# Kernel optimization log

Hardware: AMD Instinct MI355X
Metric: run time of the kernel (lower is better)

Reference implementation:

```python
import jax, jax.numpy as jnp
import numpy as np

N_NODES = 100000
N_EDGES = 20000
NNZ = 1600000


def _hconv(x, node_idx, edge_idx, W, b):
    # PyG HypergraphConv (no attention): out = D^-1 H (B^-1 H^T (x W)) + b
    xw = x @ W  # [N, F_out]
    ones = jnp.ones((node_idx.shape[0],), dtype=x.dtype)
    Bdeg = jax.ops.segment_sum(ones, edge_idx, num_segments=N_EDGES)
    Binv = jnp.where(Bdeg > 0, 1.0 / Bdeg, 0.0)
    # node -> hyperedge aggregation
    e = jax.ops.segment_sum(xw[node_idx], edge_idx, num_segments=N_EDGES)
    e = e * Binv[:, None]
    Ddeg = jax.ops.segment_sum(ones, node_idx, num_segments=N_NODES)
    Dinv = jnp.where(Ddeg > 0, 1.0 / Ddeg, 0.0)
    # hyperedge -> node aggregation
    out = jax.ops.segment_sum(e[edge_idx], node_idx, num_segments=N_NODES)
    return out * Dinv[:, None] + b


def setup_inputs() -> dict:
    key = jax.random.key(0)
    ks = jax.random.split(key, 12)
    x = jax.random.normal(ks[0], (N_NODES, 300), dtype=jnp.float32)
    node_idx = jax.random.randint(ks[1], (NNZ,), 0, N_NODES)
    edge_idx = jax.random.randint(ks[2], (NNZ,), 0, N_EDGES)
    hyper_edge_index = jnp.stack([node_idx, edge_idx], axis=0)
    def lin(kw, kb, fi, fo):
        s = 1.0 / np.sqrt(fi)
        W = jax.random.uniform(kw, (fi, fo), jnp.float32, -s, s)
        b = jax.random.uniform(kb, (fo,), jnp.float32, -s, s)
        return W, b
    W1, b1 = lin(ks[3], ks[4], 300, 256)
    W2, b2 = lin(ks[5], ks[6], 256, 256)
    W3, b3 = lin(ks[7], ks[8], 256, 128)
    attn_W, attn_b = lin(ks[9], ks[10], 128, 1)
    return {"x": x, "hyper_edge_index": hyper_edge_index,
            "W1": W1, "b1": b1, "W2": W2, "b2": b2,
            "W3": W3, "b3": b3, "attn_W": attn_W, "attn_b": attn_b}


def reference(x, hyper_edge_index, W1, b1, W2, b2, W3, b3, attn_W, attn_b):
    node_idx = hyper_edge_index[0]
    edge_idx = hyper_edge_index[1]
    h = jax.nn.leaky_relu(_hconv(x, node_idx, edge_idx, W1, b1), negative_slope=0.01)
    # dropout is identity at inference
    h = jax.nn.leaky_relu(_hconv(h, node_idx, edge_idx, W2, b2), negative_slope=0.01)
    h = _hconv(h, node_idx, edge_idx, W3, b3)  # [N, 128]
    # attention pooling over all nodes (softmax along dim 0)
    logits = h @ attn_W + attn_b  # [N, 1]
    attn = jax.nn.softmax(logits, axis=0)
    return jnp.sum(attn * h, axis=0)  # [128]
```

## Files before the change

kernel.cpp:

```cpp
#include <hip/hip_runtime.h>
#include <hip/hip_bf16.h>
#include <string.h>

#define N_NODES 100000
#define N_EDGES 20000
#define NNZ     1600000

#define CHUNK   8192
#define NBE     157
#define NBN     391
#define NBLK_BIN ((NNZ + CHUNK - 1) / CHUNK)


__device__ __forceinline__ unsigned short f2bf(float f) {
    unsigned int u = __float_as_uint(f);
    unsigned int r = (u + 0x7fffu + ((u >> 16) & 1u)) >> 16;
    return (unsigned short)r;
}
__device__ __forceinline__ float bflo(unsigned int v) { return __uint_as_float(v << 16); }
__device__ __forceinline__ float bfhi(unsigned int v) { return __uint_as_float(v & 0xffff0000u); }

__device__ __forceinline__ void async_copy16(const void* g, void* l) {
    __builtin_amdgcn_global_load_lds((const __attribute__((address_space(1))) void*)g,
                                     (__attribute__((address_space(3))) void*)l, 16, 0, 0);
}

typedef __attribute__((ext_vector_type(8))) short bf16x8;
typedef __attribute__((ext_vector_type(4))) float f32x4;


__global__ __launch_bounds__(256)
void hist_buckets(const int* __restrict__ node_idx, const int* __restrict__ edge_idx,
                  int* __restrict__ bcntE, int* __restrict__ bcntN) {
    __shared__ int hE[NBE];
    __shared__ int hN[NBN];
    int t = threadIdx.x;
    for (int i = t; i < NBE; i += 256) hE[i] = 0;
    for (int i = t; i < NBN; i += 256) hN[i] = 0;
    __syncthreads();
    long base = (long)blockIdx.x * CHUNK;
    #pragma unroll 4
    for (int k = 0; k < CHUNK / 256; k++) {
        long i = base + t + k * 256;
        if (i < NNZ) {
            atomicAdd(&hE[edge_idx[i] >> 7], 1);
            atomicAdd(&hN[node_idx[i] >> 8], 1);
        }
    }
    __syncthreads();
    for (int i = t; i < NBE; i += 256) if (hE[i]) atomicAdd(&bcntE[i], hE[i]);
    for (int i = t; i < NBN; i += 256) if (hN[i]) atomicAdd(&bcntN[i], hN[i]);
}

__global__ __launch_bounds__(512)
void small_scan(const int* __restrict__ cnt, int n,
                int* __restrict__ base, int* __restrict__ cursor) {
    __shared__ int tmp[512];
    int t = threadIdx.x;
    int v = (t < n) ? cnt[t] : 0;
    tmp[t] = v; __syncthreads();
    for (int s = 1; s < 512; s <<= 1) {
        int x = (t >= s) ? tmp[t - s] : 0;
        __syncthreads();
        tmp[t] += x;
        __syncthreads();
    }
    if (t < n) { int e = tmp[t] - v; base[t] = e; cursor[t] = e; }
    if (t == 0) base[n] = tmp[511];
}

__global__ __launch_bounds__(256)
void bin_pass(const int* __restrict__ key_idx, const int* __restrict__ val_idx,
              int kshift, int bshift, int nbuck,
              int* __restrict__ cursor, unsigned int* __restrict__ staged) {
    __shared__ int hist[512];
    __shared__ int gstart[512];
    int t = threadIdx.x;
    for (int i = t; i < nbuck; i += 256) hist[i] = 0;
    __syncthreads();
    long base = (long)blockIdx.x * CHUNK;
    for (int k = 0; k < CHUNK / 256; k++) {
        long i = base + t + k * 256;
        if (i < NNZ) atomicAdd(&hist[key_idx[i] >> bshift], 1);
    }
    __syncthreads();
    for (int i = t; i < nbuck; i += 256)
        gstart[i] = hist[i] ? atomicAdd(&cursor[i], hist[i]) : 0;
    __syncthreads();
    for (int i = t; i < nbuck; i += 256) hist[i] = 0;
    __syncthreads();
    for (int k = 0; k < CHUNK / 256; k++) {
        long i = base + t + k * 256;
        if (i < NNZ) {
            int key = key_idx[i], val = val_idx[i];
            int b = key >> bshift;
            int pos = gstart[b] + atomicAdd(&hist[b], 1);
            staged[pos] = ((unsigned int)key << kshift) | (unsigned int)val;
        }
    }
}

__global__ __launch_bounds__(256)
void build_csr(const unsigned int* __restrict__ staged, const int* __restrict__ bbase,
               int kshift, int bshift, int nkey,
               int* __restrict__ off, float* __restrict__ inv, int* __restrict__ csr) {
    __shared__ int cnt[256];
    __shared__ int cur[256];
    int b = blockIdx.x, t = threadIdx.x;
    int kpb = 1 << bshift;
    int key0 = b << bshift;
    unsigned int vmask = (1u << kshift) - 1u;
    if (t < kpb) cnt[t] = 0;
    __syncthreads();
    int s = bbase[b], e = bbase[b + 1];
    for (int j = s + t; j < e; j += 256)
        atomicAdd(&cnt[(int)(staged[j] >> kshift) - key0], 1);
    __syncthreads();
    int v = (t < kpb) ? cnt[t] : 0;
    cur[t] = v; __syncthreads();
    for (int st = 1; st < 256; st <<= 1) {
        int x = (t >= st) ? cur[t - st] : 0;
        __syncthreads();
        cur[t] += x;
        __syncthreads();
    }
    int excl = cur[t] - v;
    __syncthreads();
    if (t < kpb) {
        int key = key0 + t;
        if (key < nkey) {
            off[key] = s + excl;
            inv[key] = (v > 0) ? 1.0f / (float)v : 0.0f;
        }
        cur[t] = excl;
    }
    __syncthreads();
    for (int j = s + t; j < e; j += 256) {
        unsigned int pk = staged[j];
        int k = (int)(pk >> kshift) - key0;
        int pos = s + atomicAdd(&cur[k], 1);
        csr[pos] = (int)(pk & vmask);
    }
    if (b == 0 && t == 0) off[nkey] = NNZ;
}


__global__ void convert_pad_x(const float* __restrict__ x, unsigned short* __restrict__ xb) {
    int idx = blockIdx.x * 256 + threadIdx.x;
    if (idx < N_NODES * 320) {
        int r = idx / 320, k = idx - r * 320;
        xb[idx] = (k < 300) ? f2bf(x[(size_t)r * 300 + k]) : (unsigned short)0;
    }
}

__global__ void transpose_w(const float* __restrict__ W, unsigned short* __restrict__ Wt,
                            int K, int N, int Kp) {
    int n = blockIdx.x;
    for (int k = threadIdx.x; k < Kp; k += 256)
        Wt[(size_t)n * Kp + k] = (k < K) ? f2bf(W[(size_t)k * N + n]) : (unsigned short)0;
}


__global__ __launch_bounds__(256)
void gemm_bf16(const unsigned short* __restrict__ A,
               const unsigned short* __restrict__ Bt,
               unsigned short* __restrict__ C,
               int M, int Kp, int N) {
    __shared__ unsigned short As[128 * 32];
    __shared__ unsigned short Bs[128 * 32];
    int tid = threadIdx.x;
    int lane = tid & 63;
    int w = tid >> 6;
    int row0 = blockIdx.x * 128;
    int col0 = blockIdx.y * 128;
    int wm = w & 1, wn = w >> 1;

    f32x4 acc[4][4];
    #pragma unroll
    for (int i = 0; i < 4; i++)
        #pragma unroll
        for (int j = 0; j < 4; j++) acc[i][j] = (f32x4){0.f, 0.f, 0.f, 0.f};

    int sr = lane >> 2;
    int sc = lane & 3;

    for (int k0 = 0; k0 < Kp; k0 += 32) {
        #pragma unroll
        for (int c = 0; c < 2; c++) {
            int r = w * 32 + c * 16 + sr;
            int gr = row0 + r; if (gr >= M) gr = M - 1;
            const unsigned short* g = A + (size_t)gr * Kp + k0 + sc * 8;
            async_copy16(g, (void*)(As + (w * 32 + c * 16) * 32));
        }
        #pragma unroll
        for (int c = 0; c < 2; c++) {
            int r = w * 32 + c * 16 + sr;
            const unsigned short* g = Bt + (size_t)(col0 + r) * Kp + k0 + sc * 8;
            async_copy16(g, (void*)(Bs + (w * 32 + c * 16) * 32));
        }
        __syncthreads();

        bf16x8 a[4], b[4];
        #pragma unroll
        for (int i = 0; i < 4; i++)
            a[i] = *(const bf16x8*)(As + (wm * 64 + i * 16 + (lane & 15)) * 32 + (lane >> 4) * 8);
        #pragma unroll
        for (int j = 0; j < 4; j++)
            b[j] = *(const bf16x8*)(Bs + (wn * 64 + j * 16 + (lane & 15)) * 32 + (lane >> 4) * 8);
        #pragma unroll
        for (int i = 0; i < 4; i++)
            #pragma unroll
            for (int j = 0; j < 4; j++)
                acc[i][j] = __builtin_amdgcn_mfma_f32_16x16x32_bf16(a[i], b[j], acc[i][j], 0, 0, 0);
        __syncthreads();
    }

    int crow = (lane >> 4) * 4;
    int ccol = lane & 15;
    #pragma unroll
    for (int i = 0; i < 4; i++)
        #pragma unroll
        for (int r = 0; r < 4; r++) {
            int gr = row0 + wm * 64 + i * 16 + crow + r;
            if (gr < M) {
                #pragma unroll
                for (int j = 0; j < 4; j++) {
                    int gc = col0 + wn * 64 + j * 16 + ccol;
                    C[(size_t)gr * N + gc] = f2bf(acc[i][j][r]);
                }
            }
        }
}


__global__ void edge_agg_bf16(const unsigned short* __restrict__ X, const int* __restrict__ offE,
                              const int* __restrict__ csrE, const float* __restrict__ Binv,
                              unsigned short* __restrict__ E, int F) {
    int e = blockIdx.x;
    int f2 = threadIdx.x;
    int s = offE[e], t = offE[e + 1];
    float a0 = 0.f, a1 = 0.f;
    int j = s;
    for (; j + 3 < t; j += 4) {
        int r0 = csrE[j], r1 = csrE[j + 1], r2 = csrE[j + 2], r3 = csrE[j + 3];
        unsigned int v0 = *(const unsigned int*)(X + (size_t)r0 * F + f2 * 2);
        unsigned int v1 = *(const unsigned int*)(X + (size_t)r1 * F + f2 * 2);
        unsigned int v2 = *(const unsigned int*)(X + (size_t)r2 * F + f2 * 2);
        unsigned int v3 = *(const unsigned int*)(X + (size_t)r3 * F + f2 * 2);
        a0 += (bflo(v0) + bflo(v1)) + (bflo(v2) + bflo(v3));
        a1 += (bfhi(v0) + bfhi(v1)) + (bfhi(v2) + bfhi(v3));
    }
    for (; j < t; j++) {
        unsigned int v = *(const unsigned int*)(X + (size_t)csrE[j] * F + f2 * 2);
        a0 += bflo(v); a1 += bfhi(v);
    }
    float bi = Binv[e];
    unsigned int o = ((unsigned int)f2bf(a1 * bi) << 16) | (unsigned int)f2bf(a0 * bi);
    *(unsigned int*)(E + (size_t)e * F + f2 * 2) = o;
}

__global__ void node_agg_bf16(const unsigned short* __restrict__ Ebuf, const int* __restrict__ offN,
                              const int* __restrict__ csrN, const float* __restrict__ Dinv,
                              const float* __restrict__ bias,
                              unsigned short* __restrict__ outB, float* __restrict__ outF,
                              int F, int do_lrelu) {
    int n = blockIdx.x;
    int f2 = threadIdx.x;
    int s = offN[n], t = offN[n + 1];
    float a0 = 0.f, a1 = 0.f;
    int j = s;
    for (; j + 3 < t; j += 4) {
        int r0 = csrN[j], r1 = csrN[j + 1], r2 = csrN[j + 2], r3 = csrN[j + 3];
        unsigned int v0 = *(const unsigned int*)(Ebuf + (size_t)r0 * F + f2 * 2);
        unsigned int v1 = *(const unsigned int*)(Ebuf + (size_t)r1 * F + f2 * 2);
        unsigned int v2 = *(const unsigned int*)(Ebuf + (size_t)r2 * F + f2 * 2);
        unsigned int v3 = *(const unsigned int*)(Ebuf + (size_t)r3 * F + f2 * 2);
        a0 += (bflo(v0) + bflo(v1)) + (bflo(v2) + bflo(v3));
        a1 += (bfhi(v0) + bfhi(v1)) + (bfhi(v2) + bfhi(v3));
    }
    for (; j < t; j++) {
        unsigned int v = *(const unsigned int*)(Ebuf + (size_t)csrN[j] * F + f2 * 2);
        a0 += bflo(v); a1 += bfhi(v);
    }
    float di = Dinv[n];
    float o0 = a0 * di + bias[f2 * 2];
    float o1 = a1 * di + bias[f2 * 2 + 1];
    if (do_lrelu) {
        o0 = (o0 > 0.f) ? o0 : 0.01f * o0;
        o1 = (o1 > 0.f) ? o1 : 0.01f * o1;
    }
    if (outB) {
        unsigned int o = ((unsigned int)f2bf(o1) << 16) | (unsigned int)f2bf(o0);
        *(unsigned int*)(outB + (size_t)n * F + f2 * 2) = o;
    } else {
        outF[(size_t)n * F + f2 * 2]     = o0;
        outF[(size_t)n * F + f2 * 2 + 1] = o1;
    }
}


__global__ __launch_bounds__(256)
void logits_kernel(const float* __restrict__ H, const float* __restrict__ aW,
                   const float* __restrict__ aB, float* __restrict__ logits,
                   float* __restrict__ pmax, int N) {
    int lane = threadIdx.x & 63;
    int wave = threadIdx.x >> 6;
    int waveGlobal = blockIdx.x * 4 + wave;
    int stride = gridDim.x * 4;
    float2 w2 = ((const float2*)aW)[lane];
    float lmax = -1e30f;
    float ab = aB[0];
    for (int n = waveGlobal; n < N; n += stride) {
        float2 h2 = ((const float2*)(H + (size_t)n * 128))[lane];
        float d = h2.x * w2.x + h2.y * w2.y;
        #pragma unroll
        for (int s = 32; s > 0; s >>= 1) d += __shfl_xor(d, s, 64);
        float lg = d + ab;
        if (lane == 0) logits[n] = lg;
        lmax = fmaxf(lmax, lg);
    }
    __shared__ float wmax[4];
    if (lane == 0) wmax[wave] = lmax;
    __syncthreads();
    if (threadIdx.x == 0) {
        float m = fmaxf(fmaxf(wmax[0], wmax[1]), fmaxf(wmax[2], wmax[3]));
        pmax[blockIdx.x] = m;
    }
}

__global__ __launch_bounds__(256)
void reduce_max(const float* __restrict__ pmax, int n, float* __restrict__ gmax) {
    __shared__ float sm[256];
    float m = -1e30f;
    for (int i = threadIdx.x; i < n; i += 256) m = fmaxf(m, pmax[i]);
    sm[threadIdx.x] = m;
    __syncthreads();
    for (int s = 128; s > 0; s >>= 1) {
        if (threadIdx.x < (unsigned)s) sm[threadIdx.x] = fmaxf(sm[threadIdx.x], sm[threadIdx.x + s]);
        __syncthreads();
    }
    if (threadIdx.x == 0) *gmax = sm[0];
}

__global__ __launch_bounds__(128)
void weighted_sum(const float* __restrict__ H, const float* __restrict__ logits,
                  const float* __restrict__ gmax, float* __restrict__ gacc,
                  float* __restrict__ gsum, int N) {
    int f = threadIdx.x;
    float mx = *gmax;
    float acc = 0.f, ls = 0.f;
    for (int n = blockIdx.x; n < N; n += gridDim.x) {
        float w = __expf(logits[n] - mx);
        acc += w * H[(size_t)n * 128 + f];
        if (f == 0) ls += w;
    }
    atomicAdd(&gacc[f], acc);
    if (f == 0) atomicAdd(gsum, ls);
}

__global__ __launch_bounds__(128)
void finalize(const float* __restrict__ gacc, const float* __restrict__ gsum,
              float* __restrict__ out) {
    int f = threadIdx.x;
    out[f] = gacc[f] / gsum[0];
}


extern "C" void kernel_launch(void* const* d_in, const int* in_sizes, int n_in,
                              void* d_out, int out_size, void* d_ws, size_t ws_size,
                              hipStream_t stream) {
    const float* x        = (const float*)d_in[0];
    const int*   node_idx = (const int*)d_in[1];
    const int*   edge_idx = node_idx + NNZ;
    const float* W1 = (const float*)d_in[2];
    const float* b1 = (const float*)d_in[3];
    const float* W2 = (const float*)d_in[4];
    const float* b2 = (const float*)d_in[5];
    const float* W3 = (const float*)d_in[6];
    const float* b3 = (const float*)d_in[7];
    const float* aW = (const float*)d_in[8];
    const float* aB = (const float*)d_in[9];
    float* out = (float*)d_out;

    char* ws = (char*)d_ws;
    size_t off = 0;
    auto take = [&](size_t bytes) -> char* {
        char* r = ws + off;
        off = (off + bytes + 255) & ~(size_t)255;
        return r;
    };

    char* bcnt_base = take((size_t)(NBE + NBN) * 4);
    int* bcntE = (int*)bcnt_base;
    int* bcntN = bcntE + NBE;
    int* baseE = (int*)take((NBE + 1) * 4);
    int* baseN = (int*)take((NBN + 1) * 4);
    int* curEb = (int*)take(NBE * 4);
    int* curNb = (int*)take(NBN * 4);
    int*   offE = (int*)take((size_t)(N_EDGES + 1) * 4);
    int*   offN = (int*)take((size_t)(N_NODES + 1) * 4);
    float* Binv = (float*)take((size_t)N_EDGES * 4);
    float* Dinv = (float*)take((size_t)N_NODES * 4);
    int*   csrE = (int*)take((size_t)NNZ * 4);
    int*   csrN = (int*)take((size_t)NNZ * 4);

    unsigned short* xb  = (unsigned short*)take((size_t)N_NODES * 320 * 2);
    unsigned short* Wt1 = (unsigned short*)take((size_t)256 * 320 * 2);
    unsigned short* Wt2 = (unsigned short*)take((size_t)256 * 256 * 2);
    unsigned short* Wt3 = (unsigned short*)take((size_t)128 * 256 * 2);
    unsigned short* xw  = (unsigned short*)take((size_t)N_NODES * 256 * 2);
    unsigned short* hb  = (unsigned short*)take((size_t)N_NODES * 256 * 2);
    unsigned short* eb  = (unsigned short*)take((size_t)N_EDGES * 256 * 2);
    float* h3 = (float*)xb;

    unsigned int* stagedE = (unsigned int*)xw;
    unsigned int* stagedN = stagedE + NNZ;

    float* logits = (float*)take((size_t)N_NODES * 4);
    float* pmax   = (float*)take(400 * 4);
    char* acc_base = take((128 + 1) * 4);
    float* gacc = (float*)acc_base;
    float* gsum = gacc + 128;
    float* gmax = (float*)take(4);

    hipMemsetAsync(bcnt_base, 0, (size_t)(NBE + NBN) * 4, stream);
    hipMemsetAsync(acc_base, 0, (128 + 1) * 4, stream);

    hist_buckets<<<NBLK_BIN, 256, 0, stream>>>(node_idx, edge_idx, bcntE, bcntN);
    small_scan<<<1, 512, 0, stream>>>(bcntE, NBE, baseE, curEb);
    small_scan<<<1, 512, 0, stream>>>(bcntN, NBN, baseN, curNb);
    bin_pass<<<NBLK_BIN, 256, 0, stream>>>(edge_idx, node_idx, 17, 7, NBE, curEb, stagedE);
    bin_pass<<<NBLK_BIN, 256, 0, stream>>>(node_idx, edge_idx, 15, 8, NBN, curNb, stagedN);
    build_csr<<<NBE, 256, 0, stream>>>(stagedE, baseE, 17, 7, N_EDGES, offE, Binv, csrE);
    build_csr<<<NBN, 256, 0, stream>>>(stagedN, baseN, 15, 8, N_NODES, offN, Dinv, csrN);

    convert_pad_x<<<(N_NODES * 320 + 255) / 256, 256, 0, stream>>>(x, xb);
    transpose_w<<<256, 256, 0, stream>>>(W1, Wt1, 300, 256, 320);
    transpose_w<<<256, 256, 0, stream>>>(W2, Wt2, 256, 256, 256);
    transpose_w<<<128, 256, 0, stream>>>(W3, Wt3, 256, 128, 256);

    const int MB = (N_NODES + 127) / 128;

    gemm_bf16<<<dim3(MB, 2), 256, 0, stream>>>(xb, Wt1, xw, N_NODES, 320, 256);
    edge_agg_bf16<<<N_EDGES, 128, 0, stream>>>(xw, offE, csrE, Binv, eb, 256);
    node_agg_bf16<<<N_NODES, 128, 0, stream>>>(eb, offN, csrN, Dinv, b1, hb, nullptr, 256, 1);

    gemm_bf16<<<dim3(MB, 2), 256, 0, stream>>>(hb, Wt2, xw, N_NODES, 256, 256);
    edge_agg_bf16<<<N_EDGES, 128, 0, stream>>>(xw, offE, csrE, Binv, eb, 256);
    node_agg_bf16<<<N_NODES, 128, 0, stream>>>(eb, offN, csrN, Dinv, b2, hb, nullptr, 256, 1);

    gemm_bf16<<<dim3(MB, 1), 256, 0, stream>>>(hb, Wt3, xw, N_NODES, 256, 128);
    edge_agg_bf16<<<N_EDGES, 64, 0, stream>>>(xw, offE, csrE, Binv, eb, 128);
    node_agg_bf16<<<N_NODES, 64, 0, stream>>>(eb, offN, csrN, Dinv, b3, nullptr, h3, 128, 0);

    logits_kernel<<<400, 256, 0, stream>>>(h3, aW, aB, logits, pmax, N_NODES);
    reduce_max<<<1, 256, 0, stream>>>(pmax, 400, gmax);
    weighted_sum<<<512, 128, 0, stream>>>(h3, logits, gmax, gacc, gsum, N_NODES);
    finalize<<<1, 128, 0, stream>>>(gacc, gsum, out);
}
```

Measured before the change: 1.052 ms.

## Sort CSR segments and remap aggregation to one wave per segment chunk

Adds a bitonic sort of each CSR segment so gathered row indices are ascending, which is meant to improve cache and DRAM locality of the gathers. The edge and node aggregation kernels are rewritten to assign one 64-lane wave per segment and 128-feature chunk, packing four segments into each 256-thread block. The gather loop is unrolled to 8 loads in flight, and the fp32 output store is vectorized. Sorting adds two extra kernel launches. Segments longer than the sort buffer (256 for edges, 64 for nodes) are left unsorted, which only affects order and not correctness.

```diff
diff --git a/kernel.cpp b/kernel.cpp
--- a/kernel.cpp
+++ b/kernel.cpp
@@ -142,6 +142,30 @@
         csr[pos] = (int)(pk & vmask);
     }
     if (b == 0 && t == 0) off[nkey] = NNZ;
+}
+
+template<int MAXD>
+__global__ void sort_seg(int* __restrict__ csr, const int* __restrict__ off) {
+    __shared__ int buf[MAXD];
+    int seg = blockIdx.x;
+    int s = off[seg], e = off[seg + 1], d = e - s;
+    if (d <= 1 || d > MAXD) return;
+    for (int i = threadIdx.x; i < MAXD; i += blockDim.x)
+        buf[i] = (i < d) ? csr[s + i] : 0x7fffffff;
+    __syncthreads();
+    for (int k = 2; k <= MAXD; k <<= 1)
+        for (int j = k >> 1; j > 0; j >>= 1) {
+            for (int i = threadIdx.x; i < MAXD; i += blockDim.x) {
+                int ixj = i ^ j;
+                if (ixj > i) {
+                    int a = buf[i], b = buf[ixj];
+                    bool up = ((i & k) == 0);
+                    if ((a > b) == up) { buf[i] = b; buf[ixj] = a; }
+                }
+            }
+            __syncthreads();
+        }
+    for (int i = threadIdx.x; i < d; i += blockDim.x) csr[s + i] = buf[i];
 }
 
 
@@ -233,68 +257,79 @@
 }
 
 
-__global__ void edge_agg_bf16(const unsigned short* __restrict__ X, const int* __restrict__ offE,
-                              const int* __restrict__ csrE, const float* __restrict__ Binv,
-                              unsigned short* __restrict__ E, int F) {
-    int e = blockIdx.x;
-    int f2 = threadIdx.x;
-    int s = offE[e], t = offE[e + 1];
+__device__ __forceinline__ void seg_map(int b, int nchunk, int& chunk, int& eg) {
+    if (nchunk == 2) { chunk = (b & 7) >> 2; eg = (b >> 3) * 4 + (b & 3); }
+    else             { chunk = 0;            eg = b; }
+}
+
+__global__ __launch_bounds__(256)
+void edge_agg3(const unsigned short* __restrict__ X, const int* __restrict__ offE,
+               const int* __restrict__ csrE, const float* __restrict__ Binv,
+               unsigned short* __restrict__ E, int F, int nchunk, int nseg) {
+    int chunk, eg;
+    seg_map(blockIdx.x, nchunk, chunk, eg);
+    int wv = threadIdx.x >> 6, lane = threadIdx.x & 63;
+    int seg = eg * 4 + wv;
+    if (seg >= nseg) return;
+    int s = offE[seg], t = offE[seg + 1];
+    int stride = F >> 1;
+    const unsigned int* Xp = (const unsigned int*)X + chunk * 64 + lane;
     float a0 = 0.f, a1 = 0.f;
     int j = s;
-    for (; j + 3 < t; j += 4) {
-        int r0 = csrE[j], r1 = csrE[j + 1], r2 = csrE[j + 2], r3 = csrE[j + 3];
-        unsigned int v0 = *(const unsigned int*)(X + (size_t)r0 * F + f2 * 2);
-        unsigned int v1 = *(const unsigned int*)(X + (size_t)r1 * F + f2 * 2);
-        unsigned int v2 = *(const unsigned int*)(X + (size_t)r2 * F + f2 * 2);
-        unsigned int v3 = *(const unsigned int*)(X + (size_t)r3 * F + f2 * 2);
-        a0 += (bflo(v0) + bflo(v1)) + (bflo(v2) + bflo(v3));
-        a1 += (bfhi(v0) + bfhi(v1)) + (bfhi(v2) + bfhi(v3));
+    for (; j + 7 < t; j += 8) {
+        unsigned int v[8];
+        #pragma unroll
+        for (int q = 0; q < 8; q++) v[q] = Xp[(size_t)csrE[j + q] * stride];
+        #pragma unroll
+        for (int q = 0; q < 8; q++) { a0 += bflo(v[q]); a1 += bfhi(v[q]); }
     }
     for (; j < t; j++) {
-        unsigned int v = *(const unsigned int*)(X + (size_t)csrE[j] * F + f2 * 2);
+        unsigned int v = Xp[(size_t)csrE[j] * stride];
         a0 += bflo(v); a1 += bfhi(v);
     }
-    float bi = Binv[e];
-    unsigned int o = ((unsigned int)f2bf(a1 * bi) << 16) | (unsigned int)f2bf(a0 * bi);
-    *(unsigned int*)(E + (size_t)e * F + f2 * 2) = o;
-}
-
-__global__ void node_agg_bf16(const unsigned short* __restrict__ Ebuf, const int* __restrict__ offN,
-                              const int* __restrict__ csrN, const float* __restrict__ Dinv,
-                              const float* __restrict__ bias,
-                              unsigned short* __restrict__ outB, float* __restrict__ outF,
-                              int F, int do_lrelu) {
-    int n = blockIdx.x;
-    int f2 = threadIdx.x;
-    int s = offN[n], t = offN[n + 1];
+    float bi = Binv[seg];
+    ((unsigned int*)E)[(size_t)seg * stride + chunk * 64 + lane] =
+        ((unsigned int)f2bf(a1 * bi) << 16) | (unsigned int)f2bf(a0 * bi);
+}
+
+__global__ __launch_bounds__(256)
+void node_agg3(const unsigned short* __restrict__ Eb, const int* __restrict__ offN,
+               const int* __restrict__ csrN, const float* __restrict__ Dinv,
+               const float* __restrict__ bias, unsigned short* __restrict__ outB,
+               float* __restrict__ outF, int F, int nchunk, int nseg, int do_lrelu) {
+    int chunk, eg;
+    seg_map(blockIdx.x, nchunk, chunk, eg);
+    int wv = threadIdx.x >> 6, lane = threadIdx.x & 63;
+    int seg = eg * 4 + wv;
+    if (seg >= nseg) return;
+    int s = offN[seg], t = offN[seg + 1];
+    int stride = F >> 1;
+    const unsigned int* Ep = (const unsigned int*)Eb + chunk * 64 + lane;
     float a0 = 0.f, a1 = 0.f;
     int j = s;
-    for (; j + 3 < t; j += 4) {
-        int r0 = csrN[j], r1 = csrN[j + 1], r2 = csrN[j + 2], r3 = csrN[j + 3];
-        unsigned int v0 = *(const unsigned int*)(Ebuf + (size_t)r0 * F + f2 * 2);
-        unsigned int v1 = *(const unsigned int*)(Ebuf + (size_t)r1 * F + f2 * 2);
-        unsigned int v2 = *(const unsigned int*)(Ebuf + (size_t)r2 * F + f2 * 2);
-        unsigned int v3 = *(const unsigned int*)(Ebuf + (size_t)r3 * F + f2 * 2);
-        a0 += (bflo(v0) + bflo(v1)) + (bflo(v2) + bflo(v3));
-        a1 += (bfhi(v0) + bfhi(v1)) + (bfhi(v2) + bfhi(v3));
+    for (; j + 7 < t; j += 8) {
+        unsigned int v[8];
+        #pragma unroll
+        for (int q = 0; q < 8; q++) v[q] = Ep[(size_t)csrN[j + q] * stride];
+        #pragma unroll
+        for (int q = 0; q < 8; q++) { a0 += bflo(v[q]); a1 += bfhi(v[q]); }
     }
     for (; j < t; j++) {
-        unsigned int v = *(const unsigned int*)(Ebuf + (size_t)csrN[j] * F + f2 * 2);
+        unsigned int v = Ep[(size_t)csrN[j] * stride];
         a0 += bflo(v); a1 += bfhi(v);
     }
-    float di = Dinv[n];
-    float o0 = a0 * di + bias[f2 * 2];
-    float o1 = a1 * di + bias[f2 * 2 + 1];
+    float di = Dinv[seg];
+    float o0 = a0 * di + bias[chunk * 128 + lane * 2];
+    float o1 = a1 * di + bias[chunk * 128 + lane * 2 + 1];
     if (do_lrelu) {
         o0 = (o0 > 0.f) ? o0 : 0.01f * o0;
         o1 = (o1 > 0.f) ? o1 : 0.01f * o1;
     }
     if (outB) {
-        unsigned int o = ((unsigned int)f2bf(o1) << 16) | (unsigned int)f2bf(o0);
-        *(unsigned int*)(outB + (size_t)n * F + f2 * 2) = o;
+        ((unsigned int*)outB)[(size_t)seg * stride + chunk * 64 + lane] =
+            ((unsigned int)f2bf(o1) << 16) | (unsigned int)f2bf(o0);
     } else {
-        outF[(size_t)n * F + f2 * 2]     = o0;
-        outF[(size_t)n * F + f2 * 2 + 1] = o1;
+        ((float2*)outF)[(size_t)seg * stride + chunk * 64 + lane] = make_float2(o0, o1);
     }
 }
 
@@ -434,24 +469,29 @@
     build_csr<<<NBE, 256, 0, stream>>>(stagedE, baseE, 17, 7, N_EDGES, offE, Binv, csrE);
     build_csr<<<NBN, 256, 0, stream>>>(stagedN, baseN, 15, 8, N_NODES, offN, Dinv, csrN);
 
+    sort_seg<256><<<N_EDGES, 256, 0, stream>>>(csrE, offE);
+    sort_seg<64><<<N_NODES, 64, 0, stream>>>(csrN, offN);
+
     convert_pad_x<<<(N_NODES * 320 + 255) / 256, 256, 0, stream>>>(x, xb);
     transpose_w<<<256, 256, 0, stream>>>(W1, Wt1, 300, 256, 320);
     transpose_w<<<256, 256, 0, stream>>>(W2, Wt2, 256, 256, 256);
     transpose_w<<<128, 256, 0, stream>>>(W3, Wt3, 256, 128, 256);
 
     const int MB = (N_NODES + 127) / 128;
+    const int EG = N_EDGES / 4;
+    const int NG = N_NODES / 4;
 
     gemm_bf16<<<dim3(MB, 2), 256, 0, stream>>>(xb, Wt1, xw, N_NODES, 320, 256);
-    edge_agg_bf16<<<N_EDGES, 128, 0, stream>>>(xw, offE, csrE, Binv, eb, 256);
-    node_agg_bf16<<<N_NODES, 128, 0, stream>>>(eb, offN, csrN, Dinv, b1, hb, nullptr, 256, 1);
+    edge_agg3<<<2 * EG, 256, 0, stream>>>(xw, offE, csrE, Binv, eb, 256, 2, N_EDGES);
+    node_agg3<<<2 * NG, 256, 0, stream>>>(eb, offN, csrN, Dinv, b1, hb, nullptr, 256, 2, N_NODES, 1);
 
     gemm_bf16<<<dim3(MB, 2), 256, 0, stream>>>(hb, Wt2, xw, N_NODES, 256, 256);
-    edge_agg_bf16<<<N_EDGES, 128, 0, stream>>>(xw, offE, csrE, Binv, eb, 256);
-    node_agg_bf16<<<N_NODES, 128, 0, stream>>>(eb, offN, csrN, Dinv, b2, hb, nullptr, 256, 1);
+    edge_agg3<<<2 * EG, 256, 0, stream>>>(xw, offE, csrE, Binv, eb, 256, 2, N_EDGES);
+    node_agg3<<<2 * NG, 256, 0, stream>>>(eb, offN, csrN, Dinv, b2, hb, nullptr, 256, 2, N_NODES, 1);
 
     gemm_bf16<<<dim3(MB, 1), 256, 0, stream>>>(hb, Wt3, xw, N_NODES, 256, 128);
-    edge_agg_bf16<<<N_EDGES, 64, 0, stream>>>(xw, offE, csrE, Binv, eb, 128);
-    node_agg_bf16<<<N_NODES, 64, 0, stream>>>(eb, offN, csrN, Dinv, b3, nullptr, h3, 128, 0);
+    edge_agg3<<<EG, 256, 0, stream>>>(xw, offE, csrE, Binv, eb, 128, 1, N_EDGES);
+    node_agg3<<<NG, 256, 0, stream>>>(eb, offN, csrN, Dinv, b3, nullptr, h3, 128, 1, N_NODES, 0);
 
     logits_kernel<<<400, 256, 0, stream>>>(h3, aW, aB, logits, pmax, N_NODES);
     reduce_max<<<1, 256, 0, stream>>>(pmax, 400, gmax);
```

Result: slower. 1.247 ms (+18.5%).

## Map one wavefront per segment in edge/node aggregation with wider loads

Applied to the files above, without the earlier changes.

Replaces the one-block-per-segment aggregation kernels with kernels that assign one 64-lane wavefront per hyperedge or node, packing four segments into each 256-thread block. Each lane now loads 8 bytes (uint2) for the 256-wide layers, and the 128-wide layer unrolls by 8 gathers. The specialized kernels also drop the runtime F, lrelu and output-type branches. The aim is to cut per-block launch overhead for the 100k tiny blocks and to raise gather memory-level parallelism. The trade-off is more registers per lane and less generic code.

```diff
diff --git a/kernel.cpp b/kernel.cpp
--- a/kernel.cpp
+++ b/kernel.cpp
@@ -19,6 +19,9 @@
 }
 __device__ __forceinline__ float bflo(unsigned int v) { return __uint_as_float(v << 16); }
 __device__ __forceinline__ float bfhi(unsigned int v) { return __uint_as_float(v & 0xffff0000u); }
+__device__ __forceinline__ unsigned int packbf(float lo, float hi) {
+    return ((unsigned int)f2bf(hi) << 16) | (unsigned int)f2bf(lo);
+}
 
 __device__ __forceinline__ void async_copy16(const void* g, void* l) {
     __builtin_amdgcn_global_load_lds((const __attribute__((address_space(1))) void*)g,
@@ -233,69 +236,124 @@
 }
 
 
-__global__ void edge_agg_bf16(const unsigned short* __restrict__ X, const int* __restrict__ offE,
-                              const int* __restrict__ csrE, const float* __restrict__ Binv,
-                              unsigned short* __restrict__ E, int F) {
-    int e = blockIdx.x;
-    int f2 = threadIdx.x;
-    int s = offE[e], t = offE[e + 1];
+__global__ __launch_bounds__(256)
+void edge_agg256(const unsigned short* __restrict__ X, const int* __restrict__ off,
+                 const int* __restrict__ csr, const float* __restrict__ inv,
+                 unsigned short* __restrict__ E) {
+    int wv = threadIdx.x >> 6, lane = threadIdx.x & 63;
+    int seg = blockIdx.x * 4 + wv;
+    if (seg >= N_EDGES) return;
+    int s = off[seg], t = off[seg + 1];
+    const uint2* Xp = (const uint2*)X;
+    float a0 = 0.f, a1 = 0.f, a2 = 0.f, a3 = 0.f;
+    int j = s;
+    for (; j + 3 < t; j += 4) {
+        uint2 v[4];
+        #pragma unroll
+        for (int q = 0; q < 4; q++) v[q] = Xp[(size_t)csr[j + q] * 64 + lane];
+        #pragma unroll
+        for (int q = 0; q < 4; q++) {
+            a0 += bflo(v[q].x); a1 += bfhi(v[q].x);
+            a2 += bflo(v[q].y); a3 += bfhi(v[q].y);
+        }
+    }
+    for (; j < t; j++) {
+        uint2 v = Xp[(size_t)csr[j] * 64 + lane];
+        a0 += bflo(v.x); a1 += bfhi(v.x); a2 += bflo(v.y); a3 += bfhi(v.y);
+    }
+    float bi = inv[seg];
+    uint2 o; o.x = packbf(a0 * bi, a1 * bi); o.y = packbf(a2 * bi, a3 * bi);
+    ((uint2*)E)[(size_t)seg * 64 + lane] = o;
+}
+
+__global__ __launch_bounds__(256)
+void node_agg256(const unsigned short* __restrict__ Eb, const int* __restrict__ off,
+                 const int* __restrict__ csr, const float* __restrict__ inv,
+                 const float* __restrict__ bias, unsigned short* __restrict__ outB) {
+    int wv = threadIdx.x >> 6, lane = threadIdx.x & 63;
+    int seg = blockIdx.x * 4 + wv;
+    if (seg >= N_NODES) return;
+    int s = off[seg], t = off[seg + 1];
+    const uint2* Ep = (const uint2*)Eb;
+    float a0 = 0.f, a1 = 0.f, a2 = 0.f, a3 = 0.f;
+    int j = s;
+    for (; j + 3 < t; j += 4) {
+        uint2 v[4];
+        #pragma unroll
+        for (int q = 0; q < 4; q++) v[q] = Ep[(size_t)csr[j + q] * 64 + lane];
+        #pragma unroll
+        for (int q = 0; q < 4; q++) {
+            a0 += bflo(v[q].x); a1 += bfhi(v[q].x);
+            a2 += bflo(v[q].y); a3 += bfhi(v[q].y);
+        }
+    }
+    for (; j < t; j++) {
+        uint2 v = Ep[(size_t)csr[j] * 64 + lane];
+        a0 += bflo(v.x); a1 += bfhi(v.x); a2 += bflo(v.y); a3 += bfhi(v.y);
+    }
+    float di = inv[seg];
+    float4 b4 = ((const float4*)bias)[lane];
+    float o0 = a0 * di + b4.x, o1 = a1 * di + b4.y;
+    float o2 = a2 * di + b4.z, o3 = a3 * di + b4.w;
+    o0 = (o0 > 0.f) ? o0 : 0.01f * o0;
+    o1 = (o1 > 0.f) ? o1 : 0.01f * o1;
+    o2 = (o2 > 0.f) ? o2 : 0.01f * o2;
+    o3 = (o3 > 0.f) ? o3 : 0.01f * o3;
+    uint2 o; o.x = packbf(o0, o1); o.y = packbf(o2, o3);
+    ((uint2*)outB)[(size_t)seg * 64 + lane] = o;
+}
+
+__global__ __launch_bounds__(256)
+void edge_agg128(const unsigned short* __restrict__ X, const int* __restrict__ off,
+                 const int* __restrict__ csr, const float* __restrict__ inv,
+                 unsigned short* __restrict__ E) {
+    int wv = threadIdx.x >> 6, lane = threadIdx.x & 63;
+    int seg = blockIdx.x * 4 + wv;
+    if (seg >= N_EDGES) return;
+    int s = off[seg], t = off[seg + 1];
+    const unsigned int* Xp = (const unsigned int*)X;
     float a0 = 0.f, a1 = 0.f;
     int j = s;
-    for (; j + 3 < t; j += 4) {
-        int r0 = csrE[j], r1 = csrE[j + 1], r2 = csrE[j + 2], r3 = csrE[j + 3];
-        unsigned int v0 = *(const unsigned int*)(X + (size_t)r0 * F + f2 * 2);
-        unsigned int v1 = *(const unsigned int*)(X + (size_t)r1 * F + f2 * 2);
-        unsigned int v2 = *(const unsigned int*)(X + (size_t)r2 * F + f2 * 2);
-        unsigned int v3 = *(const unsigned int*)(X + (size_t)r3 * F + f2 * 2);
-        a0 += (bflo(v0) + bflo(v1)) + (bflo(v2) + bflo(v3));
-        a1 += (bfhi(v0) + bfhi(v1)) + (bfhi(v2) + bfhi(v3));
+    for (; j + 7 < t; j += 8) {
+        unsigned int v[8];
+        #pragma unroll
+        for (int q = 0; q < 8; q++) v[q] = Xp[(size_t)csr[j + q] * 64 + lane];
+        #pragma unroll
+        for (int q = 0; q < 8; q++) { a0 += bflo(v[q]); a1 += bfhi(v[q]); }
     }
     for (; j < t; j++) {
-        unsigned int v = *(const unsigned int*)(X + (size_t)csrE[j] * F + f2 * 2);
+        unsigned int v = Xp[(size_t)csr[j] * 64 + lane];
         a0 += bflo(v); a1 += bfhi(v);
     }
-    float bi = Binv[e];
-    unsigned int o = ((unsigned int)f2bf(a1 * bi) << 16) | (unsigned int)f2bf(a0 * bi);
-    *(unsigned int*)(E + (size_t)e * F + f2 * 2) = o;
-}
-
-__global__ void node_agg_bf16(const unsigned short* __restrict__ Ebuf, const int* __restrict__ offN,
-                              const int* __restrict__ csrN, const float* __restrict__ Dinv,
-                              const float* __restrict__ bias,
-                              unsigned short* __restrict__ outB, float* __restrict__ outF,
-                              int F, int do_lrelu) {
-    int n = blockIdx.x;
-    int f2 = threadIdx.x;
-    int s = offN[n], t = offN[n + 1];
+    float bi = inv[seg];
+    ((unsigned int*)E)[(size_t)seg * 64 + lane] = packbf(a0 * bi, a1 * bi);
+}
+
+__global__ __launch_bounds__(256)
+void node_agg128f(const unsigned short* __restrict__ Eb, const int* __restrict__ off,
+                  const int* __restrict__ csr, const float* __restrict__ inv,
+                  const float* __restrict__ bias, float* __restrict__ outF) {
+    int wv = threadIdx.x >> 6, lane = threadIdx.x & 63;
+    int seg = blockIdx.x * 4 + wv;
+    if (seg >= N_NODES) return;
+    int s = off[seg], t = off[seg + 1];
+    const unsigned int* Ep = (const unsigned int*)Eb;
     float a0 = 0.f, a1 = 0.f;
     int j = s;
-    for (; j + 3 < t; j += 4) {
-        int r0 = csrN[j], r1 = csrN[j + 1], r2 = csrN[j + 2], r3 = csrN[j + 3];
-        unsigned int v0 = *(const unsigned int*)(Ebuf + (size_t)r0 * F + f2 * 2);
-        unsigned int v1 = *(const unsigned int*)(Ebuf + (size_t)r1 * F + f2 * 2);
-        unsigned int v2 = *(const unsigned int*)(Ebuf + (size_t)r2 * F + f2 * 2);
-        unsigned int v3 = *(const unsigned int*)(Ebuf + (size_t)r3 * F + f2 * 2);
-        a0 += (bflo(v0) + bflo(v1)) + (bflo(v2) + bflo(v3));
-        a1 += (bfhi(v0) + bfhi(v1)) + (bfhi(v2) + bfhi(v3));
+    for (; j + 7 < t; j += 8) {
+        unsigned int v[8];
+        #pragma unroll
+        for (int q = 0; q < 8; q++) v[q] = Ep[(size_t)csr[j + q] * 64 + lane];
+        #pragma unroll
+        for (int q = 0; q < 8; q++) { a0 += bflo(v[q]); a1 += bfhi(v[q]); }
     }
     for (; j < t; j++) {
-        unsigned int v = *(const unsigned int*)(Ebuf + (size_t)csrN[j] * F + f2 * 2);
+        unsigned int v = Ep[(size_t)csr[j] * 64 + lane];
         a0 += bflo(v); a1 += bfhi(v);
     }
-    float di = Dinv[n];
-    float o0 = a0 * di + bias[f2 * 2];
-    float o1 = a1 * di + bias[f2 * 2 + 1];
-    if (do_lrelu) {
-        o0 = (o0 > 0.f) ? o0 : 0.01f * o0;
-        o1 = (o1 > 0.f) ? o1 : 0.01f * o1;
-    }
-    if (outB) {
-        unsigned int o = ((unsigned int)f2bf(o1) << 16) | (unsigned int)f2bf(o0);
-        *(unsigned int*)(outB + (size_t)n * F + f2 * 2) = o;
-    } else {
-        outF[(size_t)n * F + f2 * 2]     = o0;
-        outF[(size_t)n * F + f2 * 2 + 1] = o1;
-    }
+    float di = inv[seg];
+    float2 b2 = ((const float2*)bias)[lane];
+    ((float2*)outF)[(size_t)seg * 64 + lane] = make_float2(a0 * di + b2.x, a1 * di + b2.y);
 }
 
 
@@ -440,18 +498,20 @@
     transpose_w<<<128, 256, 0, stream>>>(W3, Wt3, 256, 128, 256);
 
     const int MB = (N_NODES + 127) / 128;
+    const int EB = N_EDGES / 4;
+    const int NB = N_NODES / 4;
 
     gemm_bf16<<<dim3(MB, 2), 256, 0, stream>>>(xb, Wt1, xw, N_NODES, 320, 256);
-    edge_agg_bf16<<<N_EDGES, 128, 0, stream>>>(xw, offE, csrE, Binv, eb, 256);
-    node_agg_bf16<<<N_NODES, 128, 0, stream>>>(eb, offN, csrN, Dinv, b1, hb, nullptr, 256, 1);
+    edge_agg256<<<EB, 256, 0, stream>>>(xw, offE, csrE, Binv, eb);
+    node_agg256<<<NB, 256, 0, stream>>>(eb, offN, csrN, Dinv, b1, hb);
 
     gemm_bf16<<<dim3(MB, 2), 256, 0, stream>>>(hb, Wt2, xw, N_NODES, 256, 256);
-    edge_agg_bf16<<<N_EDGES, 128, 0, stream>>>(xw, offE, csrE, Binv, eb, 256);
-    node_agg_bf16<<<N_NODES, 128, 0, stream>>>(eb, offN, csrN, Dinv, b2, hb, nullptr, 256, 1);
+    edge_agg256<<<EB, 256, 0, stream>>>(xw, offE, csrE, Binv, eb);
+    node_agg256<<<NB, 256, 0, stream>>>(eb, offN, csrN, Dinv, b2, hb);
 
     gemm_bf16<<<dim3(MB, 1), 256, 0, stream>>>(hb, Wt3, xw, N_NODES, 256, 128);
-    edge_agg_bf16<<<N_EDGES, 64, 0, stream>>>(xw, offE, csrE, Binv, eb, 128);
-    node_agg_bf16<<<N_NODES, 64, 0, stream>>>(eb, offN, csrN, Dinv, b3, nullptr, h3, 128, 0);
+    edge_agg128<<<EB, 256, 0, stream>>>(xw, offE, csrE, Binv, eb);
+    node_agg128f<<<NB, 256, 0, stream>>>(eb, offN, csrN, Dinv, b3, h3);
 
     logits_kernel<<<400, 256, 0, stream>>>(h3, aW, aB, logits, pmax, N_NODES);
     reduce_max<<<1, 256, 0, stream>>>(pmax, 400, gmax);
```

Result: no change. 1.048 ms (-0.4%).
